# Performance work log

Measured on AMD Instinct MI355X. Metric: run time of the kernel, lower is better.

Reference implementation:

```python
import jax, jax.numpy as jnp
import numpy as np

L = 2        # rnn_layers
H = 512      # hidden size
T_MAX = 20   # text_max_len
V = 10000    # NUM_WORDS
B = 32       # batch
S = 49       # spatial positions (7x7)


def setup_inputs() -> dict:
    key = jax.random.key(0)
    ks = jax.random.split(key, 12)
    w = lambda k, shape: jax.random.normal(k, shape, dtype=jnp.float32) * 0.02
    return {
        "img_channels": jax.random.normal(ks[0], (B, 512, 7, 7), dtype=jnp.float32),
        "pooled": jax.random.normal(ks[1], (B, H), dtype=jnp.float32),
        "embed_table": w(ks[2], (V, H)),
        "Wq": w(ks[3], (H, H)), "bq": jnp.zeros((H,), jnp.float32),
        "Wk": w(ks[4], (S, S)), "bk": jnp.zeros((S,), jnp.float32),
        "Wv": w(ks[5], (S, S)), "bv": jnp.zeros((S,), jnp.float32),
        "Wih": w(ks[6], (L, 4 * H, H)), "Whh": w(ks[7], (L, 4 * H, H)),
        "bih": jnp.zeros((L, 4 * H), jnp.float32), "bhh": jnp.zeros((L, 4 * H), jnp.float32),
        "projW": w(ks[8], (V, H)), "projb": jnp.zeros((V,), jnp.float32),
        "hattW": w(ks[9], (H, 2 * H)), "hattb": jnp.zeros((H,), jnp.float32),
        "sos_idx": 1,
    }


def _lstm_cell(x, h, c, wih, whh, bi, bh):
    # PyTorch gate order: i, f, g, o
    g = x @ wih.T + bi + h @ whh.T + bh
    i, f, gg, o = jnp.split(g, 4, axis=-1)
    c2 = jax.nn.sigmoid(f) * c + jax.nn.sigmoid(i) * jnp.tanh(gg)
    return jax.nn.sigmoid(o) * jnp.tanh(c2), c2


def reference(img_channels, pooled, embed_table, Wq, bq, Wk, bk, Wv, bv,
              Wih, Whh, bih, bhh, projW, projb, hattW, hattb, sos_idx):
    Bsz = img_channels.shape[0]
    chan = img_channels.reshape(Bsz, 512, -1)           # [B,512,49]
    # keys/values are step-invariant: precompute once
    keys = jnp.tanh(chan @ Wk.T + bk)                    # [B,512,49]
    values = jnp.tanh(chan @ Wv.T + bv)                  # [B,512,49]

    emb0 = jnp.broadcast_to(embed_table[sos_idx], (Bsz, H))   # <SOS> embedding
    h0 = jnp.broadcast_to(pooled[None], (L, Bsz, H))
    c0 = h0

    def step(carry, _):
        emb, h, c = carry
        x = emb
        hs, cs = [], []
        for l in range(L):  # small fixed layer count
            hl, cl = _lstm_cell(x, h[l], c[l], Wih[l], Whh[l], bih[l], bhh[l])
            hs.append(hl); cs.append(cl)
            x = hl
        out = x                                          # [B,H] top-layer output
        h = jnp.stack(hs); c = jnp.stack(cs)
        # greedy next-token embedding (no teacher forcing)
        logits = out @ projW.T + projb                   # [B,V]
        emb_next = embed_table[jnp.argmax(logits, axis=-1)]
        # cross-attention gated hidden update (all layers at once)
        q = jnp.tanh(h @ Wq.T + bq)                      # [L,B,H]
        scores = jnp.einsum('lbd,bds->lbs', q, keys) / 7.0
        w = jax.nn.softmax(scores, axis=-1)              # [L,B,49]
        attn = jnp.einsum('lbs,bds->lbd', w, values)     # [L,B,H]
        h = jnp.tanh(jnp.concatenate([attn, h], axis=-1) @ hattW.T + hattb)
        return (emb_next, h, c), out

    _, outs = jax.lax.scan(step, (emb0, h0, c0), None, length=T_MAX - 1)
    pred = jnp.concatenate([emb0[None], outs], axis=0)   # [T,B,H]
    res = jnp.einsum('tbd,vd->bvt', pred, projW) + projb[None, :, None]
    return res                                           # [B,V,T]
```

## Files before the change

### kernel.cpp

```cpp
#include <hip/hip_runtime.h>

namespace {

constexpr int B = 32, H = 512, L = 2, T = 20, V = 10000, S = 49;

__device__ __forceinline__ float sigf(float x) { return 1.0f / (1.0f + expf(-x)); }
__device__ __forceinline__ float dot4(float4 a, float4 b) {
  return a.x*b.x + a.y*b.y + a.z*b.z + a.w*b.w;
}

__global__ __launch_bounds__(256) void kv_kernel(
    const float* __restrict__ chan,
    const float* __restrict__ Wk, const float* __restrict__ bk,
    const float* __restrict__ Wv, const float* __restrict__ bv,
    float* __restrict__ keysT, float* __restrict__ valuesT) {
  __shared__ float ch[64][52];
  __shared__ float wk[49][52], wv[49][52];
  int b = blockIdx.x >> 3, dt = blockIdx.x & 7;
  int tid = threadIdx.x;
  for (int i = tid; i < 49 * 49; i += 256) {
    int s = i / 49, j = i % 49;
    wk[s][j] = Wk[i]; wv[s][j] = Wv[i];
  }
  for (int i = tid; i < 64 * 49; i += 256) {
    int d = i / 49, j = i % 49;
    ch[d][j] = chan[((size_t)b * 512 + dt * 64 + d) * S + j];
  }
  __syncthreads();
  int dl = tid >> 2, sq = tid & 3;
  for (int s = sq; s < S; s += 4) {
    float ak = bk[s], av = bv[s];
    for (int j = 0; j < 49; ++j) {
      float cv = ch[dl][j];
      ak += cv * wk[s][j];
      av += cv * wv[s][j];
    }
    int d = dt * 64 + dl;
    keysT[((size_t)b * S + s) * H + d] = tanhf(ak);
    valuesT[((size_t)b * S + s) * H + d] = tanhf(av);
  }
}

__global__ void init_kernel(const float* __restrict__ pooled,
                            const float* __restrict__ embed,
                            const int* __restrict__ sos,
                            float* __restrict__ emb, float* __restrict__ h,
                            float* __restrict__ c) {
  int idx = blockIdx.x * 256 + threadIdx.x;
  float p = pooled[idx & (B * H - 1)];
  h[idx] = p;
  c[idx] = p;
  if (idx < B * H) emb[idx] = embed[sos[0] * H + (idx & (H - 1))];
}

__global__ __launch_bounds__(256) void lstm_kernel(
    const float* __restrict__ x, const float* __restrict__ hprev,
    const float* __restrict__ cprev,
    const float* __restrict__ Wih, const float* __restrict__ Whh,
    const float* __restrict__ bih, const float* __restrict__ bhh,
    float* __restrict__ hout, float* __restrict__ cout) {
  __shared__ __align__(16) float smem[32 * 512];
  int tid = threadIdx.x;
  int hi = blockIdx.x;
  int ko = tid & 15, rr = (tid >> 4) & 3, bh = tid >> 6;

  {
    const float4* xg = (const float4*)x;
    float4* s4 = (float4*)smem;
    for (int i = tid; i < 4096; i += 256) s4[i] = xg[i];
  }
  __syncthreads();

  float acc[8];
#pragma unroll
  for (int j = 0; j < 8; ++j) acc[j] = 0.f;
  {
    const float* wrow = Wih + ((size_t)rr * H + hi) * H;
    float4 w[8];
#pragma unroll
    for (int kk = 0; kk < 8; ++kk) w[kk] = *(const float4*)&wrow[kk * 64 + ko * 4];
#pragma unroll
    for (int j = 0; j < 8; ++j) {
      const float* xb = smem + (bh * 8 + j) * 512;
#pragma unroll
      for (int kk = 0; kk < 8; ++kk)
        acc[j] += dot4(*(const float4*)&xb[kk * 64 + ko * 4], w[kk]);
    }
  }
  __syncthreads();
  {
    const float4* hg = (const float4*)hprev;
    float4* s4 = (float4*)smem;
    for (int i = tid; i < 4096; i += 256) s4[i] = hg[i];
  }
  __syncthreads();
  {
    const float* wrow = Whh + ((size_t)rr * H + hi) * H;
    float4 w[8];
#pragma unroll
    for (int kk = 0; kk < 8; ++kk) w[kk] = *(const float4*)&wrow[kk * 64 + ko * 4];
#pragma unroll
    for (int j = 0; j < 8; ++j) {
      const float* xb = smem + (bh * 8 + j) * 512;
#pragma unroll
      for (int kk = 0; kk < 8; ++kk)
        acc[j] += dot4(*(const float4*)&xb[kk * 64 + ko * 4], w[kk]);
    }
  }
  __syncthreads();

#pragma unroll
  for (int j = 0; j < 8; ++j) {
    acc[j] += __shfl_xor(acc[j], 1);
    acc[j] += __shfl_xor(acc[j], 2);
    acc[j] += __shfl_xor(acc[j], 4);
    acc[j] += __shfl_xor(acc[j], 8);
  }
  float* gbuf = smem;
  if (ko == 0) {
    float bias = bih[rr * H + hi] + bhh[rr * H + hi];
#pragma unroll
    for (int j = 0; j < 8; ++j) gbuf[rr * 32 + bh * 8 + j] = acc[j] + bias;
  }
  __syncthreads();
  if (tid < 32) {
    int b = tid;
    float gi = gbuf[b], gf = gbuf[32 + b], gg = gbuf[64 + b], go = gbuf[96 + b];
    float c2 = sigf(gf) * cprev[b * H + hi] + sigf(gi) * tanhf(gg);
    hout[b * H + hi] = sigf(go) * tanhf(c2);
    cout[b * H + hi] = c2;
  }
}

__global__ __launch_bounds__(256) void projq_kernel(
    const float* __restrict__ xin,
    const float* __restrict__ projW, const float* __restrict__ projb,
    float* __restrict__ logits, float* __restrict__ ocol, int direct, int tcol,
    const float* __restrict__ hmid_all, const float* __restrict__ Wq,
    const float* __restrict__ bq, float* __restrict__ q) {
  __shared__ __align__(16) float xs[32 * 512];
  int blk = blockIdx.x, tid = threadIdx.x;
  int ko = tid & 15, vl = tid >> 4;

  if (blk < 625) {
    {
      const float4* xg = (const float4*)xin;
      float4* s4 = (float4*)xs;
      for (int i = tid; i < 4096; i += 256) s4[i] = xg[i];
    }
    __syncthreads();
    int v = blk * 16 + vl;
    const float* wrow = projW + (size_t)v * H;
    float4 w[8];
#pragma unroll
    for (int kk = 0; kk < 8; ++kk) w[kk] = *(const float4*)&wrow[kk * 64 + ko * 4];
    float acc[32];
#pragma unroll
    for (int b = 0; b < 32; ++b) acc[b] = 0.f;
    for (int b = 0; b < 32; ++b) {
      const float* xb = xs + b * 512;
#pragma unroll
      for (int kk = 0; kk < 8; ++kk)
        acc[b] += dot4(*(const float4*)&xb[kk * 64 + ko * 4], w[kk]);
    }
#pragma unroll
    for (int b = 0; b < 32; ++b) {
      acc[b] += __shfl_xor(acc[b], 1);
      acc[b] += __shfl_xor(acc[b], 2);
      acc[b] += __shfl_xor(acc[b], 4);
      acc[b] += __shfl_xor(acc[b], 8);
    }
    if (ko == 0) {
      float bias = projb[v];
      for (int b = 0; b < 32; ++b) {
        float r = acc[b] + bias;
        logits[b * V + v] = r;
        if (direct) ocol[((size_t)b * V + v) * T + tcol] = r;
        else        ocol[b * V + v] = r;
      }
    }
  } else {
    int b2 = blk - 625;
    int lg = b2 & 1, jg = b2 >> 1;
    {
      const float4* xg = (const float4*)(hmid_all + lg * 32 * H);
      float4* s4 = (float4*)xs;
      for (int i = tid; i < 4096; i += 256) s4[i] = xg[i];
    }
    __syncthreads();
    int j = jg * 16 + vl;
    const float* wrow = Wq + (size_t)j * H;
    float4 w[8];
#pragma unroll
    for (int kk = 0; kk < 8; ++kk) w[kk] = *(const float4*)&wrow[kk * 64 + ko * 4];
    float acc[32];
#pragma unroll
    for (int b = 0; b < 32; ++b) acc[b] = 0.f;
    for (int b = 0; b < 32; ++b) {
      const float* xb = xs + b * 512;
#pragma unroll
      for (int kk = 0; kk < 8; ++kk)
        acc[b] += dot4(*(const float4*)&xb[kk * 64 + ko * 4], w[kk]);
    }
#pragma unroll
    for (int b = 0; b < 32; ++b) {
      acc[b] += __shfl_xor(acc[b], 1);
      acc[b] += __shfl_xor(acc[b], 2);
      acc[b] += __shfl_xor(acc[b], 4);
      acc[b] += __shfl_xor(acc[b], 8);
    }
    if (ko == 0) {
      float bias = bq[j];
      for (int b = 0; b < 32; ++b)
        q[(lg * 32 + b) * H + j] = tanhf(acc[b] + bias);
    }
  }
}

__global__ __launch_bounds__(256) void sattn_kernel(
    const float* __restrict__ q, const float* __restrict__ keysT,
    const float* __restrict__ valuesT, const float* __restrict__ hmid,
    float* __restrict__ cat) {
  __shared__ __align__(16) float qv[528];
  __shared__ float scl[64];
  __shared__ float wts[64];
  int lb = blockIdx.x, tid = threadIdx.x;
  int b = lb & 31;
  {
    int c0 = tid, c1 = tid + 256;
    qv[(c0 >> 7) * 132 + (c0 & 127)] = q[lb * H + c0];
    qv[(c1 >> 7) * 132 + (c1 & 127)] = q[lb * H + c1];
  }
  __syncthreads();
  int kq = tid & 3, sl = tid >> 2;
  float acc = 0.f;
  if (sl < S) {
    const float* kr = keysT + ((size_t)b * S + sl) * H + kq * 128;
    const float* qr = &qv[kq * 132];
    for (int k = 0; k < 128; k += 4)
      acc += dot4(*(const float4*)&qr[k], *(const float4*)&kr[k]);
  }
  acc += __shfl_xor(acc, 1);
  acc += __shfl_xor(acc, 2);
  if (kq == 0 && sl < S) scl[sl] = acc * (1.0f / 7.0f);
  __syncthreads();
  if (tid < 64) {
    float sc = (tid < S) ? scl[tid] : -3.4e38f;
    float m = sc;
    for (int o = 32; o > 0; o >>= 1) m = fmaxf(m, __shfl_xor(m, o));
    float e = (tid < S) ? expf(sc - m) : 0.f;
    float sum = e;
    for (int o = 32; o > 0; o >>= 1) sum += __shfl_xor(sum, o);
    if (tid < S) wts[tid] = e / sum;
  }
  __syncthreads();
  float acc0 = 0.f, acc1 = 0.f;
  for (int s = 0; s < S; ++s) {
    float w = wts[s];
    const float* vr = valuesT + ((size_t)b * S + s) * H;
    acc0 += w * vr[tid];
    acc1 += w * vr[tid + 256];
  }
  cat[lb * 1024 + tid] = acc0;
  cat[lb * 1024 + tid + 256] = acc1;
  cat[lb * 1024 + 512 + tid] = hmid[lb * H + tid];
  cat[lb * 1024 + 768 + tid] = hmid[lb * H + tid + 256];
}

__global__ __launch_bounds__(256) void hattarg_kernel(
    const float* __restrict__ cat, const float* __restrict__ hattW,
    const float* __restrict__ hattb, float* __restrict__ h,
    const float* __restrict__ logits, const float* __restrict__ embed,
    float* __restrict__ emb) {
  __shared__ __align__(16) float smem[16 * 1024];
  int blk = blockIdx.x, tid = threadIdx.x;
  if (blk < 128) {
    int lbg = blk & 3, jg = blk >> 2;
    {
      const float4* cg = (const float4*)(cat + lbg * 16 * 1024);
      float4* s4 = (float4*)smem;
      for (int i = tid; i < 4096; i += 256) s4[i] = cg[i];
    }
    __syncthreads();
    int ko = tid & 15, jl = tid >> 4;
    int j = jg * 16 + jl;
    const float* wrow = hattW + (size_t)j * 1024;
    float4 w[16];
#pragma unroll
    for (int kk = 0; kk < 16; ++kk) w[kk] = *(const float4*)&wrow[kk * 64 + ko * 4];
    float acc[16];
#pragma unroll
    for (int lb = 0; lb < 16; ++lb) acc[lb] = 0.f;
    for (int lb = 0; lb < 16; ++lb) {
      const float* cb = smem + lb * 1024;
#pragma unroll
      for (int kk = 0; kk < 16; ++kk)
        acc[lb] += dot4(*(const float4*)&cb[kk * 64 + ko * 4], w[kk]);
    }
#pragma unroll
    for (int lb = 0; lb < 16; ++lb) {
      acc[lb] += __shfl_xor(acc[lb], 1);
      acc[lb] += __shfl_xor(acc[lb], 2);
      acc[lb] += __shfl_xor(acc[lb], 4);
      acc[lb] += __shfl_xor(acc[lb], 8);
    }
    if (ko == 0) {
      float bias = hattb[j];
      for (int lb = 0; lb < 16; ++lb)
        h[(lbg * 16 + lb) * H + j] = tanhf(acc[lb] + bias);
    }
  } else {
    int b = blk - 128;
    float* sv = smem;
    int* si = (int*)(smem + 256);
    float best = -3.4e38f;
    int bi = 0x7fffffff;
    for (int it = 0; it < 10; ++it) {
      int v0 = it * 1024 + tid * 4;
      if (v0 < V) {
        float4 lv = *(const float4*)&logits[b * V + v0];
        if (lv.x > best) { best = lv.x; bi = v0; }
        if (lv.y > best) { best = lv.y; bi = v0 + 1; }
        if (lv.z > best) { best = lv.z; bi = v0 + 2; }
        if (lv.w > best) { best = lv.w; bi = v0 + 3; }
      }
    }
    sv[tid] = best; si[tid] = bi;
    __syncthreads();
    for (int st = 128; st > 0; st >>= 1) {
      if (tid < st) {
        float ov = sv[tid + st]; int oi = si[tid + st];
        if (ov > sv[tid] || (ov == sv[tid] && oi < si[tid])) { sv[tid] = ov; si[tid] = oi; }
      }
      __syncthreads();
    }
    int idx = si[0];
    for (int i = tid; i < H; i += 256) emb[b * H + i] = embed[(size_t)idx * H + i];
  }
}

__global__ __launch_bounds__(256) void finalize_kernel(
    const float* __restrict__ slog, float* __restrict__ outp) {
  int idx = blockIdx.x * 256 + threadIdx.x;
  float vals[T];
#pragma unroll
  for (int t = 0; t < T; ++t) vals[t] = slog[(size_t)t * (B * V) + idx];
#pragma unroll
  for (int t = 0; t < T; t += 4)
    *(float4*)&outp[(size_t)idx * T + t] =
        make_float4(vals[t], vals[t + 1], vals[t + 2], vals[t + 3]);
}

}

extern "C" void kernel_launch(void* const* d_in, const int* in_sizes, int n_in,
                              void* d_out, int out_size, void* d_ws, size_t ws_size,
                              hipStream_t stream) {
  const float* chan   = (const float*)d_in[0];
  const float* pooled = (const float*)d_in[1];
  const float* embed  = (const float*)d_in[2];
  const float* Wq     = (const float*)d_in[3];
  const float* bq     = (const float*)d_in[4];
  const float* Wk     = (const float*)d_in[5];
  const float* bk     = (const float*)d_in[6];
  const float* Wv     = (const float*)d_in[7];
  const float* bv     = (const float*)d_in[8];
  const float* Wih    = (const float*)d_in[9];
  const float* Whh    = (const float*)d_in[10];
  const float* bih    = (const float*)d_in[11];
  const float* bhh    = (const float*)d_in[12];
  const float* projW  = (const float*)d_in[13];
  const float* projb  = (const float*)d_in[14];
  const float* hattW  = (const float*)d_in[15];
  const float* hattb  = (const float*)d_in[16];
  const int*   sos    = (const int*)d_in[17];

  float* out = (float*)d_out;
  float* ws  = (float*)d_ws;

  float* keysT   = ws;
  float* valuesT = keysT + B * S * 512;
  float* emb     = valuesT + B * S * 512;
  float* h       = emb + B * H;
  float* c       = h + L * B * H;
  float* hmid    = c + L * B * H;
  float* cat     = hmid + L * B * H;
  float* q       = cat + L * B * 1024;
  float* logits  = q + L * B * H;
  float* slog    = logits + B * V;

  size_t base_floats = (size_t)(slog - ws);
  bool staged = ws_size >= (base_floats + (size_t)T * B * V) * sizeof(float);

  kv_kernel<<<256, 256, 0, stream>>>(chan, Wk, bk, Wv, bv, keysT, valuesT);
  init_kernel<<<(L * B * H) / 256, 256, 0, stream>>>(pooled, embed, sos, emb, h, c);
  {
    float* oc = staged ? slog : out;
    projq_kernel<<<625, 256, 0, stream>>>(emb, projW, projb, logits, oc,
                                          staged ? 0 : 1, 0,
                                          hmid, Wq, bq, q);
  }

  for (int t = 0; t < T - 1; ++t) {
    float* oc = staged ? (slog + (size_t)(t + 1) * B * V) : out;
    lstm_kernel<<<512, 256, 0, stream>>>(emb, h, c, Wih, Whh, bih, bhh, hmid, c);
    lstm_kernel<<<512, 256, 0, stream>>>(hmid, h + B * H, c + B * H,
                                         Wih + 4 * H * H, Whh + 4 * H * H,
                                         bih + 4 * H, bhh + 4 * H,
                                         hmid + B * H, c + B * H);
    projq_kernel<<<689, 256, 0, stream>>>(hmid + B * H, projW, projb, logits, oc,
                                          staged ? 0 : 1, t + 1,
                                          hmid, Wq, bq, q);
    sattn_kernel<<<L * B, 256, 0, stream>>>(q, keysT, valuesT, hmid, cat);
    hattarg_kernel<<<160, 256, 0, stream>>>(cat, hattW, hattb, h,
                                            logits, embed, emb);
  }

  if (staged) finalize_kernel<<<(B * V) / 256, 256, 0, stream>>>(slog, out);
}
```

Baseline: 1.983 ms.

## Drop LDS activation staging, read activations from cache, regroup attention/argmax kernels

The LSTM, projection/query and hidden-attention GEMV kernels no longer stage the 64KB activation matrix in shared memory. They read it straight from global memory, where it should stay cache-resident, which removes the staging copies and barriers and lifts the LDS limit on blocks per CU. The LSTM kernel fuses the Wih and Whh dot products into one loop. The argmax moves into the attention kernel, and the hatt GEMV now runs as a separate 256-block kernel. The risk is more global/L2 traffic per block in place of LDS reads.

Measured after the change: 2.398 ms. 20.9% more time.

```diff
diff --git a/kernel.cpp b/kernel.cpp
--- a/kernel.cpp
+++ b/kernel.cpp
@@ -59,56 +59,32 @@
     const float* __restrict__ Wih, const float* __restrict__ Whh,
     const float* __restrict__ bih, const float* __restrict__ bhh,
     float* __restrict__ hout, float* __restrict__ cout) {
-  __shared__ __align__(16) float smem[32 * 512];
+  __shared__ float gbuf[128];
   int tid = threadIdx.x;
   int hi = blockIdx.x;
   int ko = tid & 15, rr = (tid >> 4) & 3, bh = tid >> 6;
-
-  {
-    const float4* xg = (const float4*)x;
-    float4* s4 = (float4*)smem;
-    for (int i = tid; i < 4096; i += 256) s4[i] = xg[i];
-  }
-  __syncthreads();
-
+  const float* wihr = Wih + ((size_t)rr * H + hi) * H + ko * 4;
+  const float* whhr = Whh + ((size_t)rr * H + hi) * H + ko * 4;
+  float4 wi[8], wh[8];
+#pragma unroll
+  for (int kk = 0; kk < 8; ++kk) {
+    wi[kk] = *(const float4*)&wihr[kk * 64];
+    wh[kk] = *(const float4*)&whhr[kk * 64];
+  }
   float acc[8];
 #pragma unroll
-  for (int j = 0; j < 8; ++j) acc[j] = 0.f;
-  {
-    const float* wrow = Wih + ((size_t)rr * H + hi) * H;
-    float4 w[8];
-#pragma unroll
-    for (int kk = 0; kk < 8; ++kk) w[kk] = *(const float4*)&wrow[kk * 64 + ko * 4];
-#pragma unroll
-    for (int j = 0; j < 8; ++j) {
-      const float* xb = smem + (bh * 8 + j) * 512;
-#pragma unroll
-      for (int kk = 0; kk < 8; ++kk)
-        acc[j] += dot4(*(const float4*)&xb[kk * 64 + ko * 4], w[kk]);
-    }
-  }
-  __syncthreads();
-  {
-    const float4* hg = (const float4*)hprev;
-    float4* s4 = (float4*)smem;
-    for (int i = tid; i < 4096; i += 256) s4[i] = hg[i];
-  }
-  __syncthreads();
-  {
-    const float* wrow = Whh + ((size_t)rr * H + hi) * H;
-    float4 w[8];
-#pragma unroll
-    for (int kk = 0; kk < 8; ++kk) w[kk] = *(const float4*)&wrow[kk * 64 + ko * 4];
-#pragma unroll
-    for (int j = 0; j < 8; ++j) {
-      const float* xb = smem + (bh * 8 + j) * 512;
-#pragma unroll
-      for (int kk = 0; kk < 8; ++kk)
-        acc[j] += dot4(*(const float4*)&xb[kk * 64 + ko * 4], w[kk]);
-    }
-  }
-  __syncthreads();
-
+  for (int j = 0; j < 8; ++j) {
+    int b = bh * 8 + j;
+    const float* xb = x + (size_t)b * H + ko * 4;
+    const float* hb = hprev + (size_t)b * H + ko * 4;
+    float a = 0.f;
+#pragma unroll
+    for (int kk = 0; kk < 8; ++kk) {
+      a += dot4(*(const float4*)&xb[kk * 64], wi[kk]);
+      a += dot4(*(const float4*)&hb[kk * 64], wh[kk]);
+    }
+    acc[j] = a;
+  }
 #pragma unroll
   for (int j = 0; j < 8; ++j) {
     acc[j] += __shfl_xor(acc[j], 1);
@@ -116,7 +92,6 @@
     acc[j] += __shfl_xor(acc[j], 4);
     acc[j] += __shfl_xor(acc[j], 8);
   }
-  float* gbuf = smem;
   if (ko == 0) {
     float bias = bih[rr * H + hi] + bhh[rr * H + hi];
 #pragma unroll
@@ -138,30 +113,22 @@
     float* __restrict__ logits, float* __restrict__ ocol, int direct, int tcol,
     const float* __restrict__ hmid_all, const float* __restrict__ Wq,
     const float* __restrict__ bq, float* __restrict__ q) {
-  __shared__ __align__(16) float xs[32 * 512];
   int blk = blockIdx.x, tid = threadIdx.x;
   int ko = tid & 15, vl = tid >> 4;
-
   if (blk < 625) {
-    {
-      const float4* xg = (const float4*)xin;
-      float4* s4 = (float4*)xs;
-      for (int i = tid; i < 4096; i += 256) s4[i] = xg[i];
-    }
-    __syncthreads();
     int v = blk * 16 + vl;
-    const float* wrow = projW + (size_t)v * H;
+    const float* wrow = projW + (size_t)v * H + ko * 4;
     float4 w[8];
 #pragma unroll
-    for (int kk = 0; kk < 8; ++kk) w[kk] = *(const float4*)&wrow[kk * 64 + ko * 4];
+    for (int kk = 0; kk < 8; ++kk) w[kk] = *(const float4*)&wrow[kk * 64];
     float acc[32];
-#pragma unroll
-    for (int b = 0; b < 32; ++b) acc[b] = 0.f;
     for (int b = 0; b < 32; ++b) {
-      const float* xb = xs + b * 512;
+      const float* xb = xin + (size_t)b * H + ko * 4;
+      float a = 0.f;
 #pragma unroll
       for (int kk = 0; kk < 8; ++kk)
-        acc[b] += dot4(*(const float4*)&xb[kk * 64 + ko * 4], w[kk]);
+        a += dot4(*(const float4*)&xb[kk * 64], w[kk]);
+      acc[b] = a;
     }
 #pragma unroll
     for (int b = 0; b < 32; ++b) {
@@ -182,25 +149,19 @@
   } else {
     int b2 = blk - 625;
     int lg = b2 & 1, jg = b2 >> 1;
-    {
-      const float4* xg = (const float4*)(hmid_all + lg * 32 * H);
-      float4* s4 = (float4*)xs;
-      for (int i = tid; i < 4096; i += 256) s4[i] = xg[i];
-    }
-    __syncthreads();
     int j = jg * 16 + vl;
-    const float* wrow = Wq + (size_t)j * H;
+    const float* wrow = Wq + (size_t)j * H + ko * 4;
     float4 w[8];
 #pragma unroll
-    for (int kk = 0; kk < 8; ++kk) w[kk] = *(const float4*)&wrow[kk * 64 + ko * 4];
+    for (int kk = 0; kk < 8; ++kk) w[kk] = *(const float4*)&wrow[kk * 64];
     float acc[32];
-#pragma unroll
-    for (int b = 0; b < 32; ++b) acc[b] = 0.f;
     for (int b = 0; b < 32; ++b) {
-      const float* xb = xs + b * 512;
+      const float* xb = hmid_all + ((size_t)lg * 32 + b) * H + ko * 4;
+      float a = 0.f;
 #pragma unroll
       for (int kk = 0; kk < 8; ++kk)
-        acc[b] += dot4(*(const float4*)&xb[kk * 64 + ko * 4], w[kk]);
+        a += dot4(*(const float4*)&xb[kk * 64], w[kk]);
+      acc[b] = a;
     }
 #pragma unroll
     for (int b = 0; b < 32; ++b) {
@@ -212,105 +173,66 @@
     if (ko == 0) {
       float bias = bq[j];
       for (int b = 0; b < 32; ++b)
-        q[(lg * 32 + b) * H + j] = tanhf(acc[b] + bias);
-    }
-  }
-}
-
-__global__ __launch_bounds__(256) void sattn_kernel(
+        q[((size_t)lg * 32 + b) * H + j] = tanhf(acc[b] + bias);
+    }
+  }
+}
+
+__global__ __launch_bounds__(256) void sattnarg_kernel(
     const float* __restrict__ q, const float* __restrict__ keysT,
     const float* __restrict__ valuesT, const float* __restrict__ hmid,
-    float* __restrict__ cat) {
-  __shared__ __align__(16) float qv[528];
-  __shared__ float scl[64];
-  __shared__ float wts[64];
-  int lb = blockIdx.x, tid = threadIdx.x;
-  int b = lb & 31;
-  {
-    int c0 = tid, c1 = tid + 256;
-    qv[(c0 >> 7) * 132 + (c0 & 127)] = q[lb * H + c0];
-    qv[(c1 >> 7) * 132 + (c1 & 127)] = q[lb * H + c1];
-  }
-  __syncthreads();
-  int kq = tid & 3, sl = tid >> 2;
-  float acc = 0.f;
-  if (sl < S) {
-    const float* kr = keysT + ((size_t)b * S + sl) * H + kq * 128;
-    const float* qr = &qv[kq * 132];
-    for (int k = 0; k < 128; k += 4)
-      acc += dot4(*(const float4*)&qr[k], *(const float4*)&kr[k]);
-  }
-  acc += __shfl_xor(acc, 1);
-  acc += __shfl_xor(acc, 2);
-  if (kq == 0 && sl < S) scl[sl] = acc * (1.0f / 7.0f);
-  __syncthreads();
-  if (tid < 64) {
-    float sc = (tid < S) ? scl[tid] : -3.4e38f;
-    float m = sc;
-    for (int o = 32; o > 0; o >>= 1) m = fmaxf(m, __shfl_xor(m, o));
-    float e = (tid < S) ? expf(sc - m) : 0.f;
-    float sum = e;
-    for (int o = 32; o > 0; o >>= 1) sum += __shfl_xor(sum, o);
-    if (tid < S) wts[tid] = e / sum;
-  }
-  __syncthreads();
-  float acc0 = 0.f, acc1 = 0.f;
-  for (int s = 0; s < S; ++s) {
-    float w = wts[s];
-    const float* vr = valuesT + ((size_t)b * S + s) * H;
-    acc0 += w * vr[tid];
-    acc1 += w * vr[tid + 256];
-  }
-  cat[lb * 1024 + tid] = acc0;
-  cat[lb * 1024 + tid + 256] = acc1;
-  cat[lb * 1024 + 512 + tid] = hmid[lb * H + tid];
-  cat[lb * 1024 + 768 + tid] = hmid[lb * H + tid + 256];
-}
-
-__global__ __launch_bounds__(256) void hattarg_kernel(
-    const float* __restrict__ cat, const float* __restrict__ hattW,
-    const float* __restrict__ hattb, float* __restrict__ h,
+    float* __restrict__ cat,
     const float* __restrict__ logits, const float* __restrict__ embed,
     float* __restrict__ emb) {
-  __shared__ __align__(16) float smem[16 * 1024];
+  __shared__ __align__(16) float smem[656];
   int blk = blockIdx.x, tid = threadIdx.x;
-  if (blk < 128) {
-    int lbg = blk & 3, jg = blk >> 2;
+  if (blk < 64) {
+    float* qv = smem;
+    float* scl = smem + 528;
+    float* wts = smem + 592;
+    int lb = blk;
+    int b = lb & 31;
     {
-      const float4* cg = (const float4*)(cat + lbg * 16 * 1024);
-      float4* s4 = (float4*)smem;
-      for (int i = tid; i < 4096; i += 256) s4[i] = cg[i];
+      int c0 = tid, c1 = tid + 256;
+      qv[(c0 >> 7) * 132 + (c0 & 127)] = q[lb * H + c0];
+      qv[(c1 >> 7) * 132 + (c1 & 127)] = q[lb * H + c1];
     }
     __syncthreads();
-    int ko = tid & 15, jl = tid >> 4;
-    int j = jg * 16 + jl;
-    const float* wrow = hattW + (size_t)j * 1024;
-    float4 w[16];
-#pragma unroll
-    for (int kk = 0; kk < 16; ++kk) w[kk] = *(const float4*)&wrow[kk * 64 + ko * 4];
-    float acc[16];
-#pragma unroll
-    for (int lb = 0; lb < 16; ++lb) acc[lb] = 0.f;
-    for (int lb = 0; lb < 16; ++lb) {
-      const float* cb = smem + lb * 1024;
-#pragma unroll
-      for (int kk = 0; kk < 16; ++kk)
-        acc[lb] += dot4(*(const float4*)&cb[kk * 64 + ko * 4], w[kk]);
-    }
-#pragma unroll
-    for (int lb = 0; lb < 16; ++lb) {
-      acc[lb] += __shfl_xor(acc[lb], 1);
-      acc[lb] += __shfl_xor(acc[lb], 2);
-      acc[lb] += __shfl_xor(acc[lb], 4);
-      acc[lb] += __shfl_xor(acc[lb], 8);
-    }
-    if (ko == 0) {
-      float bias = hattb[j];
-      for (int lb = 0; lb < 16; ++lb)
-        h[(lbg * 16 + lb) * H + j] = tanhf(acc[lb] + bias);
-    }
+    int kq = tid & 3, sl = tid >> 2;
+    float acc = 0.f;
+    if (sl < S) {
+      const float* kr = keysT + ((size_t)b * S + sl) * H + kq * 128;
+      const float* qr = &qv[kq * 132];
+      for (int k = 0; k < 128; k += 4)
+        acc += dot4(*(const float4*)&qr[k], *(const float4*)&kr[k]);
+    }
+    acc += __shfl_xor(acc, 1);
+    acc += __shfl_xor(acc, 2);
+    if (kq == 0 && sl < S) scl[sl] = acc * (1.0f / 7.0f);
+    __syncthreads();
+    if (tid < 64) {
+      float sc = (tid < S) ? scl[tid] : -3.4e38f;
+      float m = sc;
+      for (int o = 32; o > 0; o >>= 1) m = fmaxf(m, __shfl_xor(m, o));
+      float e = (tid < S) ? expf(sc - m) : 0.f;
+      float sum = e;
+      for (int o = 32; o > 0; o >>= 1) sum += __shfl_xor(sum, o);
+      if (tid < S) wts[tid] = e / sum;
+    }
+    __syncthreads();
+    float acc0 = 0.f, acc1 = 0.f;
+    for (int s = 0; s < S; ++s) {
+      float w = wts[s];
+      const float* vr = valuesT + ((size_t)b * S + s) * H;
+      acc0 += w * vr[tid];
+      acc1 += w * vr[tid + 256];
+    }
+    cat[lb * 1024 + tid] = acc0;
+    cat[lb * 1024 + tid + 256] = acc1;
+    cat[lb * 1024 + 512 + tid] = hmid[lb * H + tid];
+    cat[lb * 1024 + 768 + tid] = hmid[lb * H + tid + 256];
   } else {
-    int b = blk - 128;
+    int b = blk - 64;
     float* sv = smem;
     int* si = (int*)(smem + 256);
     float best = -3.4e38f;
@@ -336,6 +258,41 @@
     }
     int idx = si[0];
     for (int i = tid; i < H; i += 256) emb[b * H + i] = embed[(size_t)idx * H + i];
+  }
+}
+
+__global__ __launch_bounds__(256) void hatt_kernel(
+    const float* __restrict__ cat, const float* __restrict__ hattW,
+    const float* __restrict__ hattb, float* __restrict__ h) {
+  int blk = blockIdx.x, tid = threadIdx.x;
+  int lbg = blk & 7, jg = blk >> 3;
+  int ko = tid & 15, jl = tid >> 4;
+  int j = jg * 16 + jl;
+  const float* wrow = hattW + (size_t)j * 1024 + ko * 4;
+  float4 w[16];
+#pragma unroll
+  for (int kk = 0; kk < 16; ++kk) w[kk] = *(const float4*)&wrow[kk * 64];
+  float acc[8];
+#pragma unroll
+  for (int lb = 0; lb < 8; ++lb) {
+    const float* cb = cat + ((size_t)lbg * 8 + lb) * 1024 + ko * 4;
+    float a = 0.f;
+#pragma unroll
+    for (int kk = 0; kk < 16; ++kk)
+      a += dot4(*(const float4*)&cb[kk * 64], w[kk]);
+    acc[lb] = a;
+  }
+#pragma unroll
+  for (int lb = 0; lb < 8; ++lb) {
+    acc[lb] += __shfl_xor(acc[lb], 1);
+    acc[lb] += __shfl_xor(acc[lb], 2);
+    acc[lb] += __shfl_xor(acc[lb], 4);
+    acc[lb] += __shfl_xor(acc[lb], 8);
+  }
+  if (ko == 0) {
+    float bias = hattb[j];
+    for (int lb = 0; lb < 8; ++lb)
+      h[((size_t)lbg * 8 + lb) * H + j] = tanhf(acc[lb] + bias);
   }
 }
 
@@ -390,15 +347,14 @@
   float* slog    = logits + B * V;
 
   size_t base_floats = (size_t)(slog - ws);
-  bool staged = ws_size >= (base_floats + (size_t)T * B * V) * sizeof(float);
+  int staged = ws_size >= (base_floats + (size_t)T * B * V) * sizeof(float) ? 1 : 0;
 
   kv_kernel<<<256, 256, 0, stream>>>(chan, Wk, bk, Wv, bv, keysT, valuesT);
   init_kernel<<<(L * B * H) / 256, 256, 0, stream>>>(pooled, embed, sos, emb, h, c);
   {
     float* oc = staged ? slog : out;
     projq_kernel<<<625, 256, 0, stream>>>(emb, projW, projb, logits, oc,
-                                          staged ? 0 : 1, 0,
-                                          hmid, Wq, bq, q);
+                                          staged ? 0 : 1, 0, hmid, Wq, bq, q);
   }
 
   for (int t = 0; t < T - 1; ++t) {
@@ -409,11 +365,10 @@
                                          bih + 4 * H, bhh + 4 * H,
                                          hmid + B * H, c + B * H);
     projq_kernel<<<689, 256, 0, stream>>>(hmid + B * H, projW, projb, logits, oc,
-                                          staged ? 0 : 1, t + 1,
-                                          hmid, Wq, bq, q);
-    sattn_kernel<<<L * B, 256, 0, stream>>>(q, keysT, valuesT, hmid, cat);
-    hattarg_kernel<<<160, 256, 0, stream>>>(cat, hattW, hattb, h,
+                                          staged ? 0 : 1, t + 1, hmid, Wq, bq, q);
+    sattnarg_kernel<<<96, 256, 0, stream>>>(q, keysT, valuesT, hmid, cat,
                                             logits, embed, emb);
+    hatt_kernel<<<256, 256, 0, stream>>>(cat, hattW, hattb, h);
   }
 
   if (staged) finalize_kernel<<<(B * V) / 256, 256, 0, stream>>>(slog, out);
```
